# Kernel tuning notes

Hardware: AMD Instinct MI355X
Metric: run time of the kernel (lower is better)

The kernel has to match this reference:

```python
import jax, jax.numpy as jnp
import numpy as np

D_MODEL = 1024
M = 4
NUM_EXPERTS = 8
TOP_K = 2
B, T = 2, 2048


def setup_inputs() -> dict:
    key = jax.random.key(0)
    ks = jax.random.split(key, 4)
    d_ff = D_MODEL * M
    x = jax.random.normal(ks[0], (B, T, D_MODEL), dtype=jnp.float32)
    # torch nn.Linear(d_model, num_experts, bias=False): stored here as (D, E) so logits = x @ gate_w
    gate_w = jax.random.normal(ks[1], (D_MODEL, NUM_EXPERTS), dtype=jnp.float32) * 0.02
    w1 = jax.random.normal(ks[2], (NUM_EXPERTS, D_MODEL, d_ff), dtype=jnp.float32) * 0.02
    b1 = jnp.zeros((NUM_EXPERTS, d_ff), dtype=jnp.float32)
    w2 = jax.random.normal(ks[3], (NUM_EXPERTS, d_ff, D_MODEL), dtype=jnp.float32) * 0.02
    b2 = jnp.zeros((NUM_EXPERTS, D_MODEL), dtype=jnp.float32)
    return {"x": x, "gate_w": gate_w, "w1": w1, "b1": b1, "w2": w2, "b2": b2}


def reference(x, gate_w, w1, b1, w2, b2):
    Bb, Tt, D = x.shape
    E = w1.shape[0]
    N = Bb * Tt
    # gating: top-k logits -> softmax over the k selected experts
    logits = jnp.einsum('btd,de->bte', x, gate_w)               # (B,T,E)
    top_v, top_i = jax.lax.top_k(logits, TOP_K)                 # (B,T,K)
    top_w = jax.nn.softmax(top_v, axis=-1)                      # (B,T,K)

    xf = x.reshape(N, D)
    idx = top_i.reshape(N, TOP_K)
    wts = top_w.reshape(N, TOP_K)
    # dense combine weights: comb[n, e] = sum_k wts[n,k] * [idx[n,k]==e]
    comb = jnp.zeros((N, E), dtype=x.dtype).at[jnp.arange(N)[:, None], idx].add(wts)

    # per-expert dense 2-layer MLP (exact erf GELU, matching torch F.gelu default),
    # combined with gate weights (zero weight == token not routed to expert).
    out = jnp.zeros((N, D), dtype=x.dtype)
    for e in range(E):
        h = jax.nn.gelu(xf @ w1[e] + b1[e], approximate=False)  # (N, D*M)
        out = out + comb[:, e:e + 1] * (h @ w2[e] + b2[e])      # (N, D)
    return out.reshape(Bb, Tt, D)
```

## Files before the change

### kernel.cpp

```cpp
#include <hip/hip_runtime.h>
#include <hip/hip_bf16.h>
#include <math.h>

#define D_MODEL 1024
#define D_FF    4096
#define NEXP    8
#define NTOK    4096
#define NROUTED 8192
#define MAXJOBS 40

typedef __attribute__((ext_vector_type(8))) short bf16x8;
typedef __attribute__((ext_vector_type(4))) float f32x4;
typedef __attribute__((ext_vector_type(4))) unsigned short us4;

#define WS_CNT   0
#define WS_CNT2  64
#define WS_OFF   128
#define WS_JOBS  192
#define WS_TI    512
#define WS_TW    (WS_TI + NTOK*2*4)
#define WS_TOK   (WS_TW + NTOK*2*4)
#define WS_GWT   (WS_TOK + NROUTED*4)
#define WS_XG    (((WS_GWT + NROUTED*4) + 255) & ~255)
#define WS_H     (WS_XG + (size_t)NROUTED*D_MODEL*2)
#define WS_WT    (WS_H + (size_t)NROUTED*D_FF*2)
#define WS_WT2   (WS_WT + (size_t)NEXP*D_FF*D_MODEL*2)
#define WS_END   (WS_WT2 + (size_t)NEXP*D_FF*D_MODEL*2)

__device__ __forceinline__ unsigned short f2bf(float f){
  union { float f; unsigned u; } a; a.f = f;
  unsigned u = a.u;
  u = u + 0x7FFF + ((u >> 16) & 1);
  return (unsigned short)(u >> 16);
}

__device__ __forceinline__ void gload_lds16(const void* g, void* l){
  __builtin_amdgcn_global_load_lds((const __attribute__((address_space(1))) void*)g,
                                   (__attribute__((address_space(3))) void*)l, 16, 0, 0);
}

__global__ void moe_gate_kernel(const float* __restrict__ x, const float* __restrict__ gw,
                                int* cnt, int* __restrict__ ti, float* __restrict__ tw){
  int n = blockIdx.x*4 + (threadIdx.x >> 6);
  int lane = threadIdx.x & 63;
  const float* xr = x + (size_t)n * D_MODEL;
  float acc[NEXP];
  #pragma unroll
  for (int e=0;e<NEXP;e++) acc[e] = 0.f;
  for (int d=lane; d<D_MODEL; d+=64){
    float xv = xr[d];
    #pragma unroll
    for (int e=0;e<NEXP;e++) acc[e] += xv * gw[d*NEXP + e];
  }
  #pragma unroll
  for (int e=0;e<NEXP;e++){
    #pragma unroll
    for (int o=32;o;o>>=1) acc[e] += __shfl_down(acc[e], o, 64);
  }
  if (lane == 0){
    int i0 = 0; float v0 = acc[0];
    #pragma unroll
    for (int e=1;e<NEXP;e++) if (acc[e] > v0){ v0 = acc[e]; i0 = e; }
    int i1 = -1; float v1 = -1e30f;
    #pragma unroll
    for (int e=0;e<NEXP;e++) if (e != i0 && acc[e] > v1){ v1 = acc[e]; i1 = e; }
    float p = expf(v1 - v0);
    float inv = 1.f / (1.f + p);
    ti[n*2] = i0; ti[n*2+1] = i1;
    tw[n*2] = inv; tw[n*2+1] = p * inv;
    atomicAdd(&cnt[i0], 1); atomicAdd(&cnt[i1], 1);
  }
}

__global__ void moe_prefix_kernel(const int* __restrict__ cnt, int* __restrict__ off,
                                  int* __restrict__ jobs){
  if (threadIdx.x == 0){
    int s = 0;
    for (int e=0;e<NEXP;e++){ off[e] = s; s += cnt[e]; }
    off[NEXP] = s;
    int idx = 0;
    for (int e=0;e<NEXP;e++){
      int ns = (cnt[e] + 255) >> 8;
      for (int q=0;q<ns;q++) jobs[1+idx++] = (e<<16) | q;
    }
    jobs[0] = idx;
  }
}

__device__ __forceinline__ void assign_body(
    int n, const float* __restrict__ x, const int* __restrict__ ti,
    const float* __restrict__ tw, const int* __restrict__ off,
    int* cnt2, int* __restrict__ tok, float* __restrict__ gwt,
    unsigned short* __restrict__ Xg){
  __shared__ int ss[2];
  if (threadIdx.x == 0){
    int i0 = ti[n*2], i1 = ti[n*2+1];
    int s0 = off[i0] + atomicAdd(&cnt2[i0], 1);
    int s1 = off[i1] + atomicAdd(&cnt2[i1], 1);
    tok[s0] = n; tok[s1] = n;
    gwt[s0] = tw[n*2]; gwt[s1] = tw[n*2+1];
    ss[0] = s0; ss[1] = s1;
  }
  __syncthreads();
  int s0 = ss[0], s1 = ss[1];
  int t = threadIdx.x;
  f32x4 v = *(const f32x4*)(x + (size_t)n * D_MODEL + t*4);
  us4 pk = { f2bf(v.x), f2bf(v.y), f2bf(v.z), f2bf(v.w) };
  __builtin_nontemporal_store(pk, (us4*)(Xg + (size_t)s0 * D_MODEL + t*4));
  __builtin_nontemporal_store(pk, (us4*)(Xg + (size_t)s1 * D_MODEL + t*4));
}

__device__ __forceinline__ void transpose_body(
    int idx, const float* __restrict__ W, unsigned short* __restrict__ Wt, int K, int F){
  __shared__ float tile[64][65];
  int fpe = F >> 6, kpe = K >> 6;
  int e = idx / (fpe*kpe), rem = idx % (fpe*kpe);
  int f0 = (rem % fpe) * 64, k0 = (rem / fpe) * 64;
  const float* Wb = W + (size_t)e * K * F;
  unsigned short* Wtb = Wt + (size_t)e * F * K;
  int tid = threadIdx.x;
  #pragma unroll
  for (int i=0;i<4;i++){
    int q = i*256 + tid;
    int r = q >> 4, c4 = (q & 15) * 4;
    f32x4 v = __builtin_nontemporal_load((const f32x4*)(Wb + (size_t)(k0 + r) * F + f0 + c4));
    tile[r][c4] = v.x; tile[r][c4+1] = v.y; tile[r][c4+2] = v.z; tile[r][c4+3] = v.w;
  }
  __syncthreads();
  #pragma unroll
  for (int i=0;i<4;i++){
    int q = i*256 + tid;
    int f = q >> 4, k4 = (q & 15) * 4;
    us4 pk = { f2bf(tile[k4][f]), f2bf(tile[k4+1][f]), f2bf(tile[k4+2][f]), f2bf(tile[k4+3][f]) };
    __builtin_nontemporal_store(pk, (us4*)(Wtb + (size_t)(f0 + f) * K + k0 + k4));
  }
}

__global__ void moe_assign_kernel(const float* x, const int* ti, const float* tw,
                                  const int* off, int* cnt2, int* tok, float* gwt,
                                  unsigned short* Xg){
  assign_body(blockIdx.x, x, ti, tw, off, cnt2, tok, gwt, Xg);
}
__global__ __launch_bounds__(256) void transpose_bf16_kernel(
    const float* W, unsigned short* Wt, int K, int F){
  transpose_body(blockIdx.x, W, Wt, K, F);
}

__global__ __launch_bounds__(256) void moe_fused_mid_kernel(
    const float* __restrict__ x, const int* __restrict__ ti, const float* __restrict__ tw,
    const int* __restrict__ off, int* cnt2, int* __restrict__ tok, float* __restrict__ gwt,
    unsigned short* __restrict__ Xg,
    const float* __restrict__ w1, unsigned short* __restrict__ Wt1,
    const float* __restrict__ w2, unsigned short* __restrict__ Wt2){
  int b = blockIdx.x;
  if (b < NTOK){
    assign_body(b, x, ti, tw, off, cnt2, tok, gwt, Xg);
  } else if (b < NTOK + 8192){
    transpose_body(b - NTOK, w1, Wt1, D_MODEL, D_FF);
  } else {
    transpose_body(b - NTOK - 8192, w2, Wt2, D_FF, D_MODEL);
  }
}

template<int MODE>
__global__ __launch_bounds__(1024) void moe_gemm_kernel(
    char* __restrict__ wsb, const unsigned short* __restrict__ Bt,
    const float* __restrict__ bias, float* __restrict__ out)
{
  const int* jobs = (const int*)(wsb + WS_JOBS);
  if ((int)blockIdx.y >= jobs[0]) return;
  const int jb = jobs[1 + blockIdx.y];
  const int e = jb >> 16;
  const int row0 = (jb & 0xffff) << 8;

  const int* off = (const int*)(wsb + WS_OFF);
  const int n0 = off[e];
  const int ne = off[e+1] - n0;

  constexpr int K  = (MODE==1) ? D_MODEL : D_FF;
  constexpr int NT = (MODE==1) ? 32 : 64;
  const int bx     = (MODE==1) ? blockIdx.x : (blockIdx.x & 3);
  const int kchunk = (MODE==1) ? 0 : (blockIdx.x >> 2);
  const int n_off  = bx * 256;
  const size_t kcb = (size_t)kchunk * 4096;

  const unsigned short* Ag = (const unsigned short*)(wsb + (MODE==1 ? (size_t)WS_XG : (size_t)WS_H));

  __shared__ __align__(16) char lds[3*32768];

  const int tid = threadIdx.x, lane = tid & 63, w = tid >> 6;
  const int wr = w >> 2, wc = w & 3;

  const int rA   = w*16 + (lane >> 2);
  const int qs   = ((lane & 3) ^ ((rA >> 1) & 3)) << 4;
  int grA = row0 + rA; if (grA >= ne) grA = ne - 1;
  const char* aSrc = (const char*)(Ag + (size_t)(n0 + grA) * K) + kcb + qs;
  const char* bSrc = (const char*)(Bt + (size_t)e * D_FF * D_MODEL + (size_t)(n_off + rA) * K) + kcb + qs;
  const int dA = w*1024, dB = 16384 + w*1024;

  const int q0 = lane >> 4;
  int aoff[4], boff[4];
  #pragma unroll
  for (int mi=0; mi<4; mi++){
    int row = wr*64 + mi*16 + (lane & 15);
    aoff[mi] = row*64 + ((q0 ^ ((row>>1)&3)) << 4);
  }
  #pragma unroll
  for (int ni=0; ni<4; ni++){
    int col = wc*64 + ni*16 + (lane & 15);
    boff[ni] = 16384 + col*64 + ((q0 ^ ((col>>1)&3)) << 4);
  }

  f32x4 acc[4][4];
  #pragma unroll
  for (int i=0;i<4;i++)
    #pragma unroll
    for (int j=0;j<4;j++) acc[i][j] = (f32x4){0.f,0.f,0.f,0.f};

  #define STAGE(tt, ss) { \
    gload_lds16(aSrc + (size_t)(tt)*64, lds + (ss)*32768 + dA); \
    gload_lds16(bSrc + (size_t)(tt)*64, lds + (ss)*32768 + dB); }

  STAGE(0, 0);
  STAGE(1, 1);

  for (int t = 0; t < NT; ++t){
    if (t < NT-1) asm volatile("s_waitcnt vmcnt(2)" ::: "memory");
    else          asm volatile("s_waitcnt vmcnt(0)" ::: "memory");
    __builtin_amdgcn_s_barrier();
    __builtin_amdgcn_sched_barrier(0);

    if (t + 2 < NT) STAGE(t + 2, (t + 2) % 3);

    const char* base = lds + (t % 3) * 32768;
    bf16x8 a[4], b[4];
    #pragma unroll
    for (int mi=0; mi<4; mi++) a[mi] = *(const bf16x8*)(base + aoff[mi]);
    #pragma unroll
    for (int ni=0; ni<4; ni++) b[ni] = *(const bf16x8*)(base + boff[ni]);

    asm volatile("s_waitcnt lgkmcnt(0)" ::: "memory");
    __builtin_amdgcn_sched_barrier(0);
    __builtin_amdgcn_s_setprio(1);
    #pragma unroll
    for (int ni=0; ni<4; ni++)
      #pragma unroll
      for (int mi=0; mi<4; mi++)
        acc[mi][ni] = __builtin_amdgcn_mfma_f32_16x16x32_bf16(a[mi], b[ni], acc[mi][ni], 0, 0, 0);
    __builtin_amdgcn_s_setprio(0);
    __builtin_amdgcn_sched_barrier(0);
  }
  #undef STAGE

  if (MODE == 1){
    const float* b1 = bias + (size_t)e * D_FF;
    unsigned short* H = (unsigned short*)(wsb + (size_t)WS_H);
    #pragma unroll
    for (int mi=0; mi<4; mi++){
      int rbase = wr*64 + mi*16 + ((lane>>4)<<2);
      #pragma unroll
      for (int rr=0;rr<4;rr++){
        int lrow = rbase + rr;
        if (row0 + lrow < ne){
          size_t hb = (size_t)(n0 + row0 + lrow) * D_FF;
          #pragma unroll
          for (int ni=0; ni<4; ni++){
            int gcol = n_off + wc*64 + ni*16 + (lane&15);
            float v = acc[mi][ni][rr] + b1[gcol];
            v = 0.5f * v * (1.f + erff(v * 0.70710678118654752f));
            __builtin_nontemporal_store(f2bf(v), H + hb + gcol);
          }
        }
      }
    }
  } else {
    const float* b2 = bias + (size_t)e * D_MODEL;
    const int* tok = (const int*)(wsb + WS_TOK);
    const float* gwt = (const float*)(wsb + WS_GWT);
    #pragma unroll
    for (int mi=0; mi<4; mi++){
      int rbase = wr*64 + mi*16 + ((lane>>4)<<2);
      #pragma unroll
      for (int rr=0;rr<4;rr++){
        int lrow = rbase + rr;
        if (row0 + lrow < ne){
          int slot = n0 + row0 + lrow;
          int tk = tok[slot];
          float g = gwt[slot];
          float* orow = out + (size_t)tk * D_MODEL;
          #pragma unroll
          for (int ni=0; ni<4; ni++){
            int gcol = n_off + wc*64 + ni*16 + (lane&15);
            float bb = (kchunk == 0) ? b2[gcol] : 0.f;
            atomicAdd(orow + gcol, (acc[mi][ni][rr] + bb) * g);
          }
        }
      }
    }
  }
}

extern "C" void kernel_launch(void* const* d_in, const int* in_sizes, int n_in,
                              void* d_out, int out_size, void* d_ws, size_t ws_size,
                              hipStream_t stream){
  const float* x   = (const float*)d_in[0];
  const float* gw  = (const float*)d_in[1];
  const float* w1  = (const float*)d_in[2];
  const float* b1  = (const float*)d_in[3];
  const float* w2  = (const float*)d_in[4];
  const float* b2  = (const float*)d_in[5];
  float* out = (float*)d_out;
  char* ws = (char*)d_ws;
  unsigned short* Wt1 = (unsigned short*)(ws + (size_t)WS_WT);
  unsigned short* Wt2 = (unsigned short*)(ws + (size_t)WS_WT2);

  hipMemsetAsync(ws, 0, 512, stream);
  hipMemsetAsync(out, 0, (size_t)NTOK * D_MODEL * sizeof(float), stream);

  moe_gate_kernel<<<NTOK/4, 256, 0, stream>>>(x, gw, (int*)(ws+WS_CNT),
                                              (int*)(ws+WS_TI), (float*)(ws+WS_TW));
  moe_prefix_kernel<<<1, 64, 0, stream>>>((const int*)(ws+WS_CNT), (int*)(ws+WS_OFF),
                                          (int*)(ws+WS_JOBS));

  if (ws_size >= (size_t)WS_END){
    moe_fused_mid_kernel<<<NTOK + 16384, 256, 0, stream>>>(
        x, (const int*)(ws+WS_TI), (const float*)(ws+WS_TW), (const int*)(ws+WS_OFF),
        (int*)(ws+WS_CNT2), (int*)(ws+WS_TOK), (float*)(ws+WS_GWT),
        (unsigned short*)(ws + (size_t)WS_XG), w1, Wt1, w2, Wt2);
    moe_gemm_kernel<1><<<dim3(D_FF/256, MAXJOBS), 1024, 0, stream>>>(ws, Wt1, b1, out);
    moe_gemm_kernel<2><<<dim3((D_MODEL/256)*2, MAXJOBS), 1024, 0, stream>>>(ws, Wt2, b2, out);
  } else {
    moe_assign_kernel<<<NTOK, 256, 0, stream>>>(x, (const int*)(ws+WS_TI),
                                                (const float*)(ws+WS_TW), (const int*)(ws+WS_OFF),
                                                (int*)(ws+WS_CNT2), (int*)(ws+WS_TOK),
                                                (float*)(ws+WS_GWT),
                                                (unsigned short*)(ws + (size_t)WS_XG));
    transpose_bf16_kernel<<<8192, 256, 0, stream>>>(w1, Wt1, D_MODEL, D_FF);
    moe_gemm_kernel<1><<<dim3(D_FF/256, MAXJOBS), 1024, 0, stream>>>(ws, Wt1, b1, out);
    transpose_bf16_kernel<<<8192, 256, 0, stream>>>(w2, Wt1, D_FF, D_MODEL);
    moe_gemm_kernel<2><<<dim3((D_MODEL/256)*2, MAXJOBS), 1024, 0, stream>>>(ws, Wt1, b2, out);
  }
}
```

Before: 568.2 us.

## Overlap w2 transpose with first expert GEMM via extra grid rows

Moves the w2 fp32-to-bf16 transpose out of the pre-GEMM fused kernel and into extra blocks appended to the first GEMM launch, each 1024-thread block handling four 64x64 tiles in its LDS. The first kernel now only does token assignment and the w1 transpose. The aim is to hide the memory-bound w2 conversion behind the compute-bound first GEMM instead of running it serially beforehand. The risk is that the extra blocks compete for CUs and bandwidth with the GEMM, or get scheduled after it and add a tail.

```diff
diff --git a/kernel.cpp b/kernel.cpp
--- a/kernel.cpp
+++ b/kernel.cpp
@@ -110,18 +110,17 @@
   __builtin_nontemporal_store(pk, (us4*)(Xg + (size_t)s1 * D_MODEL + t*4));
 }
 
-__device__ __forceinline__ void transpose_body(
-    int idx, const float* __restrict__ W, unsigned short* __restrict__ Wt, int K, int F){
-  __shared__ float tile[64][65];
+__device__ __forceinline__ void transpose_tile(
+    int idx, int gtid, float (*tile)[65],
+    const float* __restrict__ W, unsigned short* __restrict__ Wt, int K, int F){
   int fpe = F >> 6, kpe = K >> 6;
   int e = idx / (fpe*kpe), rem = idx % (fpe*kpe);
   int f0 = (rem % fpe) * 64, k0 = (rem / fpe) * 64;
   const float* Wb = W + (size_t)e * K * F;
   unsigned short* Wtb = Wt + (size_t)e * F * K;
-  int tid = threadIdx.x;
   #pragma unroll
   for (int i=0;i<4;i++){
-    int q = i*256 + tid;
+    int q = i*256 + gtid;
     int r = q >> 4, c4 = (q & 15) * 4;
     f32x4 v = __builtin_nontemporal_load((const f32x4*)(Wb + (size_t)(k0 + r) * F + f0 + c4));
     tile[r][c4] = v.x; tile[r][c4+1] = v.y; tile[r][c4+2] = v.z; tile[r][c4+3] = v.w;
@@ -129,44 +128,49 @@
   __syncthreads();
   #pragma unroll
   for (int i=0;i<4;i++){
-    int q = i*256 + tid;
+    int q = i*256 + gtid;
     int f = q >> 4, k4 = (q & 15) * 4;
     us4 pk = { f2bf(tile[k4][f]), f2bf(tile[k4+1][f]), f2bf(tile[k4+2][f]), f2bf(tile[k4+3][f]) };
     __builtin_nontemporal_store(pk, (us4*)(Wtb + (size_t)(f0 + f) * K + k0 + k4));
   }
 }
 
-__global__ void moe_assign_kernel(const float* x, const int* ti, const float* tw,
-                                  const int* off, int* cnt2, int* tok, float* gwt,
-                                  unsigned short* Xg){
-  assign_body(blockIdx.x, x, ti, tw, off, cnt2, tok, gwt, Xg);
-}
 __global__ __launch_bounds__(256) void transpose_bf16_kernel(
     const float* W, unsigned short* Wt, int K, int F){
-  transpose_body(blockIdx.x, W, Wt, K, F);
-}
-
-__global__ __launch_bounds__(256) void moe_fused_mid_kernel(
+  __shared__ float tile[64][65];
+  transpose_tile(blockIdx.x, threadIdx.x, tile, W, Wt, K, F);
+}
+
+__global__ __launch_bounds__(256) void moe_fusedA_kernel(
     const float* __restrict__ x, const int* __restrict__ ti, const float* __restrict__ tw,
     const int* __restrict__ off, int* cnt2, int* __restrict__ tok, float* __restrict__ gwt,
     unsigned short* __restrict__ Xg,
-    const float* __restrict__ w1, unsigned short* __restrict__ Wt1,
-    const float* __restrict__ w2, unsigned short* __restrict__ Wt2){
+    const float* __restrict__ w1, unsigned short* __restrict__ Wt1){
   int b = blockIdx.x;
   if (b < NTOK){
     assign_body(b, x, ti, tw, off, cnt2, tok, gwt, Xg);
-  } else if (b < NTOK + 8192){
-    transpose_body(b - NTOK, w1, Wt1, D_MODEL, D_FF);
   } else {
-    transpose_body(b - NTOK - 8192, w2, Wt2, D_FF, D_MODEL);
+    __shared__ float tile[64][65];
+    transpose_tile(b - NTOK, threadIdx.x, tile, w1, Wt1, D_MODEL, D_FF);
   }
 }
 
 template<int MODE>
 __global__ __launch_bounds__(1024) void moe_gemm_kernel(
     char* __restrict__ wsb, const unsigned short* __restrict__ Bt,
-    const float* __restrict__ bias, float* __restrict__ out)
+    const float* __restrict__ bias, float* __restrict__ out,
+    const float* __restrict__ w2src, unsigned short* __restrict__ Wt2)
 {
+  __shared__ __align__(16) char lds[3*32768];
+
+  if (MODE == 1 && (int)blockIdx.y >= MAXJOBS){
+    int slot = ((int)blockIdx.y - MAXJOBS) * (int)gridDim.x + (int)blockIdx.x;
+    int g = threadIdx.x >> 8, gtid = threadIdx.x & 255;
+    float (*tiles)[64][65] = (float(*)[64][65])lds;
+    transpose_tile(slot*4 + g, gtid, tiles[g], w2src, Wt2, D_FF, D_MODEL);
+    return;
+  }
+
   const int* jobs = (const int*)(wsb + WS_JOBS);
   if ((int)blockIdx.y >= jobs[0]) return;
   const int jb = jobs[1 + blockIdx.y];
@@ -185,8 +189,6 @@
   const size_t kcb = (size_t)kchunk * 4096;
 
   const unsigned short* Ag = (const unsigned short*)(wsb + (MODE==1 ? (size_t)WS_XG : (size_t)WS_H));
-
-  __shared__ __align__(16) char lds[3*32768];
 
   const int tid = threadIdx.x, lane = tid & 63, w = tid >> 6;
   const int wr = w >> 2, wc = w & 3;
@@ -321,23 +323,17 @@
                                               (int*)(ws+WS_TI), (float*)(ws+WS_TW));
   moe_prefix_kernel<<<1, 64, 0, stream>>>((const int*)(ws+WS_CNT), (int*)(ws+WS_OFF),
                                           (int*)(ws+WS_JOBS));
+  moe_fusedA_kernel<<<NTOK + 8192, 256, 0, stream>>>(
+      x, (const int*)(ws+WS_TI), (const float*)(ws+WS_TW), (const int*)(ws+WS_OFF),
+      (int*)(ws+WS_CNT2), (int*)(ws+WS_TOK), (float*)(ws+WS_GWT),
+      (unsigned short*)(ws + (size_t)WS_XG), w1, Wt1);
 
   if (ws_size >= (size_t)WS_END){
-    moe_fused_mid_kernel<<<NTOK + 16384, 256, 0, stream>>>(
-        x, (const int*)(ws+WS_TI), (const float*)(ws+WS_TW), (const int*)(ws+WS_OFF),
-        (int*)(ws+WS_CNT2), (int*)(ws+WS_TOK), (float*)(ws+WS_GWT),
-        (unsigned short*)(ws + (size_t)WS_XG), w1, Wt1, w2, Wt2);
-    moe_gemm_kernel<1><<<dim3(D_FF/256, MAXJOBS), 1024, 0, stream>>>(ws, Wt1, b1, out);
-    moe_gemm_kernel<2><<<dim3((D_MODEL/256)*2, MAXJOBS), 1024, 0, stream>>>(ws, Wt2, b2, out);
+    moe_gemm_kernel<1><<<dim3(D_FF/256, MAXJOBS + 128), 1024, 0, stream>>>(ws, Wt1, b1, out, w2, Wt2);
+    moe_gemm_kernel<2><<<dim3((D_MODEL/256)*2, MAXJOBS), 1024, 0, stream>>>(ws, Wt2, b2, out, nullptr, nullptr);
   } else {
-    moe_assign_kernel<<<NTOK, 256, 0, stream>>>(x, (const int*)(ws+WS_TI),
-                                                (const float*)(ws+WS_TW), (const int*)(ws+WS_OFF),
-                                                (int*)(ws+WS_CNT2), (int*)(ws+WS_TOK),
-                                                (float*)(ws+WS_GWT),
-                                                (unsigned short*)(ws + (size_t)WS_XG));
-    transpose_bf16_kernel<<<8192, 256, 0, stream>>>(w1, Wt1, D_MODEL, D_FF);
-    moe_gemm_kernel<1><<<dim3(D_FF/256, MAXJOBS), 1024, 0, stream>>>(ws, Wt1, b1, out);
+    moe_gemm_kernel<1><<<dim3(D_FF/256, MAXJOBS), 1024, 0, stream>>>(ws, Wt1, b1, out, nullptr, nullptr);
     transpose_bf16_kernel<<<8192, 256, 0, stream>>>(w2, Wt1, D_FF, D_MODEL);
-    moe_gemm_kernel<2><<<dim3((D_MODEL/256)*2, MAXJOBS), 1024, 0, stream>>>(ws, Wt1, b2, out);
-  }
-}
+    moe_gemm_kernel<2><<<dim3((D_MODEL/256)*2, MAXJOBS), 1024, 0, stream>>>(ws, Wt1, b2, out, nullptr, nullptr);
+  }
+}
```

Result: faster. 541.7 us (median of 2 runs) (-4.7%).
